# Kernel tuning notes

Measured on AMD Instinct MI355X. Metric: run time of the kernel, lower is better.

Reference implementation:

```python
import jax, jax.numpy as jnp
import numpy as np
from jax import lax

RPN_BBOX_STD_DEV = np.array([0.1, 0.1, 0.2, 0.2], dtype=np.float32)
PRE_NMS_LIMIT = 6000
PROPOSAL_COUNT = 1000
NMS_THRESHOLD = 0.7


def apply_box_deltas(boxes, deltas):
    # boxes: [N,4] (y1,x1,y2,x2); deltas: [N,4] (dy,dx,log dh,log dw)
    h = boxes[:, 2] - boxes[:, 0]
    w = boxes[:, 3] - boxes[:, 1]
    cy = boxes[:, 0] + 0.5 * h + deltas[:, 0] * h
    cx = boxes[:, 1] + 0.5 * w + deltas[:, 1] * w
    h = h * jnp.exp(deltas[:, 2])
    w = w * jnp.exp(deltas[:, 3])
    y1 = cy - 0.5 * h
    x1 = cx - 0.5 * w
    return jnp.stack([y1, x1, y1 + h, x1 + w], axis=1)


def pairwise_iou(boxes):
    # boxes: [N,4] -> iou [N,N]
    y1, x1, y2, x2 = boxes[:, 0], boxes[:, 1], boxes[:, 2], boxes[:, 3]
    area = (y2 - y1) * (x2 - x1)
    iy1 = jnp.maximum(y1[:, None], y1[None, :])
    ix1 = jnp.maximum(x1[:, None], x1[None, :])
    iy2 = jnp.minimum(y2[:, None], y2[None, :])
    ix2 = jnp.minimum(x2[:, None], x2[None, :])
    inter = jnp.maximum(iy2 - iy1, 0.0) * jnp.maximum(ix2 - ix1, 0.0)
    union = area[:, None] + area[None, :] - inter
    return inter / jnp.maximum(union, 1e-12)


def nms_keep_mask(boxes, iou_threshold):
    # boxes are sorted by descending score; greedy suppression.
    n = boxes.shape[0]
    iou = pairwise_iou(boxes)  # [N,N]
    idxs = jnp.arange(n)

    def body(i, keep):
        suppressed = jnp.any((iou[i] > iou_threshold) & keep & (idxs < i))
        return keep.at[i].set(jnp.logical_not(suppressed))

    return lax.fori_loop(0, n, body, jnp.zeros((n,), dtype=bool))


def proposal_single(scores, deltas, anchors):
    # scores: [A], deltas: [A,4], anchors: [A,4] -- single image
    top_scores, ix = lax.top_k(scores, PRE_NMS_LIMIT)           # sorted desc
    d = deltas[ix] * RPN_BBOX_STD_DEV[None, :]
    boxes = apply_box_deltas(anchors[ix], d)
    boxes = jnp.clip(boxes, 0.0, 1.0)                           # window [0,0,1,1]
    keep = lax.stop_gradient(nms_keep_mask(boxes, NMS_THRESHOLD))
    # select top PROPOSAL_COUNT kept boxes in score order, pad with zeros
    masked = jnp.where(keep, top_scores, -jnp.inf)
    _, sel = lax.top_k(masked, PROPOSAL_COUNT)
    valid = keep[sel]
    props = jnp.where(valid[:, None], boxes[sel], 0.0)          # [P,4]
    return props


def reference(rpn_probs, rpn_bbox, anchors):
    scores = rpn_probs[:, :, 1]  # fg prob
    return jax.vmap(proposal_single)(scores, rpn_bbox, anchors)


def setup_inputs() -> dict:
    key = jax.random.key(0)
    k1, k2, k3, k4 = jax.random.split(key, 4)
    B, A = 8, 131072
    rpn_probs = jax.random.uniform(k1, (B, A, 2), dtype=jnp.float32)
    rpn_bbox = jax.random.normal(k2, (B, A, 4), dtype=jnp.float32)
    # valid normalized anchors: y1<y2, x1<x2, inside [0,1]
    tl = jax.random.uniform(k3, (B, A, 2), dtype=jnp.float32) * 0.9
    wh = jax.random.uniform(k4, (B, A, 2), dtype=jnp.float32) * 0.1 + 1e-3
    anchors = jnp.concatenate([tl, tl + wh], axis=-1)
    return {"rpn_probs": rpn_probs, "rpn_bbox": rpn_bbox, "anchors": anchors}
```

## Files before the change

### kernel.cpp

```cpp
#include <hip/hip_runtime.h>

#pragma clang fp contract(off)

typedef unsigned long long u64;
typedef unsigned int u32;
typedef unsigned short u16;

#define BATCH 8
#define NA 131072
#define NSEL 6000
#define NT 24
#define TILE 256
#define NWORD (NT * 4)
#define NPAD (NT * TILE)
#define CAND_CAP 8192
#define PROP 1000
#define SCAP 4096
#define LDSE 12288
#define CELLCAP 256
#define LARGECAP 1024
#define LTHR 0.125f

#define OFF_HIST     0
#define OFF_BFILL    8256
#define OFF_SCNT     16512
#define OFF_CELLCNT  17344
#define MEMSET_BYTES 19456
#define OFF_TILET    19456
#define OFF_CAND     1592320
#define OFF_BOXES    2116608
#define OFF_CELLLIST 2903040
#define OFF_LARGE    3165184
#define OFF_SENT     3181568

__device__ __forceinline__ int bucket_of(u32 bits) {
  u32 hi = bits >> 16;
  if (hi >= 0x3E80u && hi < 0x3F80u) return (int)(hi - 0x3E80u);
  if (hi >= 0x3F80u && hi < 0x8000u) return 255;
  return -1;
}

__device__ __forceinline__ bool iou_gt(float4 A, float4 B, float areaA, float areaB) {
  float iy = fminf(A.z, B.z) - fmaxf(A.x, B.x);
  float ix = fminf(A.w, B.w) - fmaxf(A.y, B.y);
  float inter = fmaxf(iy, 0.0f) * fmaxf(ix, 0.0f);
  float uni = (areaA + areaB) - inter;
  float uc = fmaxf(uni, 1e-12f);
  return (double)inter >= 0x1.666667p-1 * (double)uc;
}

__device__ __forceinline__ void emit_pair(int b, int ra, int rb, u64* tileT,
                                          u32* sent, int* scnt) {
  int src = min(ra, rb), dst = max(ra, rb);
  int tsrc = src >> 8, tdst = dst >> 8;
  if (tsrc == tdst) {
    atomicOr(&tileT[(((size_t)b * NT + tdst) * TILE + (dst & 255)) * 4 + ((src >> 6) & 3)],
             1ULL << (src & 63));
  } else {
    int e = atomicAdd(&scnt[b * NT + tdst], 1);
    if (e < SCAP)
      sent[(size_t)(b * NT + tdst) * SCAP + e] = ((u32)src << 8) | (u32)(dst & 255);
  }
}

__device__ __forceinline__ u64 shfl_xor_u64(u64 v, int lanemask) {
  u32 lo = (u32)v, hi = (u32)(v >> 32);
  lo = (u32)__shfl_xor((int)lo, lanemask);
  hi = (u32)__shfl_xor((int)hi, lanemask);
  return ((u64)hi << 32) | (u64)lo;
}

__device__ __forceinline__ u64 valid_mask(int g) {
  int lo = g * 64;
  if (lo + 64 <= NSEL) return ~0ULL;
  if (lo >= NSEL) return 0ULL;
  return (1ULL << (NSEL - lo)) - 1ULL;
}

__device__ __forceinline__ void prefix_from_hist(const int* __restrict__ hist, int b,
                                                 int* h, int* bst, int* tb_s) {
  if (threadIdx.x < 256) h[threadIdx.x] = hist[b * 257 + threadIdx.x];
  __syncthreads();
  if (threadIdx.x == 0) {
    int run = 0, t = 0;
    bool found = false;
    for (int v = 255; v >= 0; --v) {
      bst[v] = run;
      run += h[v];
      if (!found && run >= NSEL) { t = v; found = true; }
    }
    *tb_s = t;
  }
  __syncthreads();
}

__global__ __launch_bounds__(256) void hist_kernel(const float* __restrict__ probs,
                                                   int* __restrict__ hist) {
  int b = blockIdx.y;
  const float2* p2 = reinterpret_cast<const float2*>(probs);
  __shared__ int h[257];
  for (int i = threadIdx.x; i < 257; i += 256) h[i] = 0;
  __syncthreads();
  int stride = gridDim.x * blockDim.x;
  for (int a = blockIdx.x * blockDim.x + threadIdx.x; a < NA; a += stride) {
    float sc = p2[(size_t)b * NA + a].y;
    int bk = bucket_of(__float_as_uint(sc));
    atomicAdd(&h[bk < 0 ? 256 : bk], 1);
  }
  __syncthreads();
  for (int i = threadIdx.x; i < 257; i += 256)
    if (h[i]) atomicAdd(&hist[b * 257 + i], h[i]);
}

__global__ __launch_bounds__(256) void gather_kernel(const float* __restrict__ probs,
                                                     const int* __restrict__ hist,
                                                     int* __restrict__ bfill,
                                                     u64* __restrict__ cand) {
  int b = blockIdx.y;
  const float2* p2 = reinterpret_cast<const float2*>(probs);
  __shared__ int h[256];
  __shared__ int bst[256];
  __shared__ int tb_s;
  prefix_from_hist(hist, b, h, bst, &tb_s);
  int tb = tb_s;
  int stride = gridDim.x * blockDim.x;
  for (int a = blockIdx.x * blockDim.x + threadIdx.x; a < NA; a += stride) {
    float sc = p2[(size_t)b * NA + a].y;
    u32 bits = __float_as_uint(sc);
    int bk = bucket_of(bits);
    if (bk >= tb) {
      int pos = bst[bk] + atomicAdd(&bfill[b * 257 + bk], 1);
      if (pos < CAND_CAP)
        cand[(size_t)b * CAND_CAP + pos] = ((u64)bits << 32) | (u64)(0xFFFFFFFFu - (u32)a);
    }
  }
}

__global__ __launch_bounds__(256) void sortdecode_kernel(const int* __restrict__ hist,
                                                         const int* __restrict__ bfill,
                                                         const u64* __restrict__ cand,
                                                         const float* __restrict__ anchors,
                                                         const float* __restrict__ deltas,
                                                         float4* __restrict__ boxes,
                                                         int* __restrict__ cellCnt,
                                                         u16* __restrict__ cellList,
                                                         u16* __restrict__ largeList,
                                                         u64* __restrict__ tileT) {
  int b = blockIdx.y;
  int tid = threadIdx.x;
  for (int g = blockIdx.x * 256 + tid; g < NT * TILE * 4; g += 64 * 256)
    tileT[(size_t)b * (NT * TILE * 4) + g] = 0ULL;
  __shared__ int h[256];
  __shared__ int bst[256];
  __shared__ int tb_s;
  prefix_from_hist(hist, b, h, bst, &tb_s);
  if (blockIdx.x == 0) {
    float4 z = {0.f, 0.f, 0.f, 0.f};
    for (int r = NSEL + tid; r < NPAD; r += 256) boxes[(size_t)b * NPAD + r] = z;
  }
  int v = tb_s + blockIdx.x;
  if (v > 255) return;
  int start = bst[v];
  if (start >= NSEL) return;
  int cnt = min(min(bfill[b * 257 + v], 1024), CAND_CAP - start);
  if (cnt <= 0) return;
  const u64* seg = cand + (size_t)b * CAND_CAP + start;
  __shared__ u64 s[1024];
  u64 x[4];
#pragma unroll
  for (int p = 0; p < 4; ++p) {
    int i = p * 256 + tid;
    x[p] = (i < cnt) ? seg[i] : 0ULL;
  }
  for (int k = 2; k <= 64; k <<= 1) {
    for (int j = k >> 1; j >= 1; j >>= 1) {
#pragma unroll
      for (int p = 0; p < 4; ++p) {
        int i = p * 256 + tid;
        u64 pv = shfl_xor_u64(x[p], j);
        bool takemax = (((i & j) == 0) == ((i & k) == 0));
        u64 mx = x[p] > pv ? x[p] : pv;
        u64 mn = x[p] < pv ? x[p] : pv;
        x[p] = takemax ? mx : mn;
      }
    }
  }
#pragma unroll
  for (int p = 0; p < 4; ++p) s[p * 256 + tid] = x[p];
  __syncthreads();
  for (int k = 128; k <= 1024; k <<= 1) {
    for (int j = k >> 1; j >= 64; j >>= 1) {
      for (int q = tid; q < 512; q += 256) {
        int i = ((q & ~(j - 1)) << 1) | (q & (j - 1));
        int ixj = i | j;
        u64 a = s[i], c = s[ixj];
        bool up = ((i & k) == 0);
        if (up ? (a < c) : (a > c)) { s[i] = c; s[ixj] = a; }
      }
      __syncthreads();
    }
#pragma unroll
    for (int p = 0; p < 4; ++p) x[p] = s[p * 256 + tid];
    for (int j = 32; j >= 1; j >>= 1) {
#pragma unroll
      for (int p = 0; p < 4; ++p) {
        int i = p * 256 + tid;
        u64 pv = shfl_xor_u64(x[p], j);
        bool takemax = (((i & j) == 0) == ((i & k) == 0));
        u64 mx = x[p] > pv ? x[p] : pv;
        u64 mn = x[p] < pv ? x[p] : pv;
        x[p] = takemax ? mx : mn;
      }
    }
    __syncthreads();
#pragma unroll
    for (int p = 0; p < 4; ++p) s[p * 256 + tid] = x[p];
    __syncthreads();
  }
  for (int i = tid; i < cnt; i += 256) {
    int r = start + i;
    if (r >= NSEL) continue;
    u64 key = s[i];
    float4 o = {0.f, 0.f, 0.f, 0.f};
    u32 idx = 0xFFFFFFFFu - (u32)(key & 0xFFFFFFFFu);
    if (idx < NA) {
      float4 av = *reinterpret_cast<const float4*>(anchors + ((size_t)b * NA + idx) * 4);
      float4 dv = *reinterpret_cast<const float4*>(deltas + ((size_t)b * NA + idx) * 4);
      float y1 = av.x, x1 = av.y, y2 = av.z, x2 = av.w;
      float dy = dv.x * 0.1f, dx = dv.y * 0.1f;
      float dh = dv.z * 0.2f, dw = dv.w * 0.2f;
      float hh = y2 - y1, ww = x2 - x1;
      float cy = y1 + 0.5f * hh + dy * hh;
      float cx = x1 + 0.5f * ww + dx * ww;
      hh = hh * expf(dh);
      ww = ww * expf(dw);
      float ny1 = cy - 0.5f * hh, nx1 = cx - 0.5f * ww;
      float ny2 = ny1 + hh, nx2 = nx1 + ww;
      o.x = fminf(fmaxf(ny1, 0.f), 1.f);
      o.y = fminf(fmaxf(nx1, 0.f), 1.f);
      o.z = fminf(fmaxf(ny2, 0.f), 1.f);
      o.w = fminf(fmaxf(nx2, 0.f), 1.f);
    }
    boxes[(size_t)b * NPAD + r] = o;
    float bh = o.z - o.x, bw = o.w - o.y;
    if (bh > LTHR || bw > LTHR) {
      int pos = atomicAdd(&cellCnt[b * 65 + 64], 1);
      if (pos < LARGECAP) largeList[b * LARGECAP + pos] = (u16)r;
    } else {
      int gy = min(7, max(0, (int)((o.x + o.z) * 4.0f)));
      int gx = min(7, max(0, (int)((o.y + o.w) * 4.0f)));
      int cell = gy * 8 + gx;
      int pos = atomicAdd(&cellCnt[b * 65 + cell], 1);
      if (pos < CELLCAP) cellList[((size_t)b * 64 + cell) * CELLCAP + pos] = (u16)r;
    }
  }
}

__global__ __launch_bounds__(256) void pairs_kernel(const float4* __restrict__ boxes,
                                                    const u16* __restrict__ cellList,
                                                    const u16* __restrict__ largeList,
                                                    const int* __restrict__ cellCnt,
                                                    u64* __restrict__ tileT,
                                                    u32* __restrict__ sent,
                                                    int* __restrict__ scnt) {
  int b = blockIdx.y;
  int tid = threadIdx.x;
  if (blockIdx.x >= 64) {
    int lb = blockIdx.x - 64;
    int nL = min(cellCnt[b * 65 + 64], LARGECAP);
    if (nL == 0) return;
    for (int li = lb; li < nL; li += 64) {
      int L = largeList[b * LARGECAP + li];
      float4 Lb = boxes[(size_t)b * NPAD + L];
      float hL = Lb.z - Lb.x, wL = Lb.w - Lb.y;
      if (0.7f * hL >= 0.126f || 0.7f * wL >= 0.126f) continue;
      float La = hL * wL;
      float sLy = Lb.x + Lb.z, sLx = Lb.y + Lb.w;
      int gy0 = max(0, (int)((sLy - 0.08f) * 4.0f));
      int gy1 = min(7, (int)((sLy + 0.08f) * 4.0f));
      int gx0 = max(0, (int)((sLx - 0.08f) * 4.0f));
      int gx1 = min(7, (int)((sLx + 0.08f) * 4.0f));
      for (int gy = gy0; gy <= gy1; ++gy)
        for (int gx = gx0; gx <= gx1; ++gx) {
          int cc = gy * 8 + gx;
          int cnt = min(cellCnt[b * 65 + cc], CELLCAP);
          for (int i = tid; i < cnt; i += 256) {
            int r = cellList[((size_t)b * 64 + cc) * CELLCAP + i];
            float4 jb = boxes[(size_t)b * NPAD + r];
            float ja = (jb.z - jb.x) * (jb.w - jb.y);
            if (iou_gt(Lb, jb, La, ja)) emit_pair(b, L, r, tileT, sent, scnt);
          }
        }
    }
    int s = 1;
    while ((1 << s) < nL) ++s;
    int tot = nL << s, m = (1 << s) - 1;
    int stride = 64 * 256;
    for (int t = lb * 256 + tid; t < tot; t += stride) {
      int i = t >> s, j = t & m;
      if (j >= nL || i >= j) continue;
      int Li = largeList[b * LARGECAP + i];
      int Lj = largeList[b * LARGECAP + j];
      float4 A = boxes[(size_t)b * NPAD + Li];
      float4 B = boxes[(size_t)b * NPAD + Lj];
      float aA = (A.z - A.x) * (A.w - A.y);
      float aB = (B.z - B.x) * (B.w - B.y);
      if (iou_gt(A, B, aA, aB)) emit_pair(b, Li, Lj, tileT, sent, scnt);
    }
    return;
  }
  int c = blockIdx.x;
  int cy = c >> 3, cx = c & 7;
  int nA = min(cellCnt[b * 65 + c], CELLCAP);
  if (nA == 0) return;
  __shared__ float4 Ab[CELLCAP];
  __shared__ float Aa[CELLCAP];
  __shared__ float Asx[CELLCAP];
  __shared__ float Asy[CELLCAP];
  __shared__ u16 Ai[CELLCAP];
  __shared__ u16 fAi[CELLCAP];
  __shared__ float4 Bb[3 * CELLCAP];
  __shared__ float Ba[3 * CELLCAP];
  __shared__ u16 Bi[3 * CELLCAP];
  __shared__ int nfA_s, nfB_s;
  for (int i = tid; i < nA; i += 256) {
    int r = cellList[((size_t)b * 64 + c) * CELLCAP + i];
    float4 bx = boxes[(size_t)b * NPAD + r];
    Ab[i] = bx;
    Aa[i] = (bx.z - bx.x) * (bx.w - bx.y);
    Asy[i] = bx.x + bx.z;
    Asx[i] = bx.y + bx.w;
    Ai[i] = (u16)r;
  }
  __syncthreads();
  {
    int totS = (nA * (nA - 1)) >> 1;
    for (int t = tid; t < totS; t += 256) {
      int i = (int)((1.0f + sqrtf(8.0f * (float)t + 1.0f)) * 0.5f);
      int tri = (i * (i - 1)) >> 1;
      if (t < tri) {
        --i;
        tri = (i * (i - 1)) >> 1;
      } else if (t >= tri + i) {
        tri += i;
        ++i;
      }
      int j = t - tri;
      if (iou_gt(Ab[i], Ab[j], Aa[i], Aa[j]))
        emit_pair(b, Ai[i], Ai[j], tileT, sent, scnt);
    }
  }
  if (cx < 7) {
    __syncthreads();
    if (tid == 0) { nfA_s = 0; nfB_s = 0; }
    __syncthreads();
    float XR2 = (float)(cx + 1) * 0.25f;
    for (int i = tid; i < nA; i += 256)
      if (Asx[i] > XR2 - 0.078f) fAi[atomicAdd(&nfA_s, 1)] = (u16)i;
    int nc = c + 1;
    int nN = min(cellCnt[b * 65 + nc], CELLCAP);
    for (int i = tid; i < nN; i += 256) {
      int r = cellList[((size_t)b * 64 + nc) * CELLCAP + i];
      float4 bx = boxes[(size_t)b * NPAD + r];
      if (bx.y + bx.w < XR2 + 0.078f) {
        int p = atomicAdd(&nfB_s, 1);
        Bb[p] = bx;
        Ba[p] = (bx.z - bx.x) * (bx.w - bx.y);
        Bi[p] = (u16)r;
      }
    }
    __syncthreads();
    int nfA = nfA_s, nfB = nfB_s;
    if (nfA && nfB) {
      int s = 1;
      while ((1 << s) < nfB) ++s;
      int tot = nfA << s, m = (1 << s) - 1;
      for (int t = tid; t < tot; t += 256) {
        int ii = fAi[t >> s], j = t & m;
        if (j < nfB && iou_gt(Ab[ii], Bb[j], Aa[ii], Ba[j]))
          emit_pair(b, Ai[ii], Bi[j], tileT, sent, scnt);
      }
    }
  }
  if (cy < 7) {
    __syncthreads();
    if (tid == 0) { nfA_s = 0; nfB_s = 0; }
    __syncthreads();
    float YB2 = (float)(cy + 1) * 0.25f;
    float XL2 = (float)cx * 0.25f;
    float XR2 = (float)(cx + 1) * 0.25f;
    for (int i = tid; i < nA; i += 256)
      if (Asy[i] > YB2 - 0.078f) fAi[atomicAdd(&nfA_s, 1)] = (u16)i;
    for (int k = 0; k < 3; ++k) {
      int nx = cx + k - 1;
      if (nx < 0 || nx > 7) continue;
      int nc = (cy + 1) * 8 + nx;
      int nN = min(cellCnt[b * 65 + nc], CELLCAP);
      for (int i = tid; i < nN; i += 256) {
        int r = cellList[((size_t)b * 64 + nc) * CELLCAP + i];
        float4 bx = boxes[(size_t)b * NPAD + r];
        float bsy = bx.x + bx.z, bsx = bx.y + bx.w;
        bool ok = bsy < YB2 + 0.078f;
        if (k == 0) ok = ok && (bsx > XL2 - 0.078f);
        if (k == 2) ok = ok && (bsx < XR2 + 0.078f);
        if (ok) {
          int p = atomicAdd(&nfB_s, 1);
          Bb[p] = bx;
          Ba[p] = (bx.z - bx.x) * (bx.w - bx.y);
          Bi[p] = (u16)r;
        }
      }
    }
    __syncthreads();
    int nfA = nfA_s, nfB = nfB_s;
    if (nfA && nfB) {
      int s = 1;
      while ((1 << s) < nfB) ++s;
      int tot = nfA << s, m = (1 << s) - 1;
      for (int t = tid; t < tot; t += 256) {
        int ii = fAi[t >> s], j = t & m;
        if (j < nfB && iou_gt(Ab[ii], Bb[j], Aa[ii], Ba[j]))
          emit_pair(b, Ai[ii], Bi[j], tileT, sent, scnt);
      }
    }
  }
}

__global__ __launch_bounds__(512) void nms_kernel(const u32* __restrict__ sent,
                                                  const int* __restrict__ scnt,
                                                  const u64* __restrict__ tileT,
                                                  const float4* __restrict__ boxes,
                                                  float4* __restrict__ out) {
  int b = blockIdx.x;
  int tid = threadIdx.x;
  int lane = tid & 63;
  int wv = tid >> 6;
  __shared__ u32 entS[LDSE];
  __shared__ u32 rmb[TILE];
  __shared__ u64 Kall[NWORD];
  __shared__ int cw[NT];
  __shared__ int prefix[NT + 1];
  __shared__ int baseT[NT];
  if (tid < NT) cw[tid] = min(scnt[b * NT + tid], SCAP);
  if (tid < TILE) rmb[tid] = 0u;
  if (tid < NWORD) Kall[tid] = 0ULL;
  {
    float4 z = {0.f, 0.f, 0.f, 0.f};
    for (int i = tid; i < PROP; i += 512) out[(size_t)b * PROP + i] = z;
  }
  __syncthreads();
  if (tid == 0) {
    int run = 0;
    for (int t = 0; t < NT; ++t) { prefix[t] = run; run += cw[t]; }
    prefix[NT] = run;
  }
  __syncthreads();
  for (int t = wv; t < NT; t += 8) {
    const u32* gb = sent + (size_t)(b * NT + t) * SCAP;
    int base = prefix[t], n = cw[t];
    for (int e = lane; e < n; e += 64) {
      int slot = base + e;
      if (slot < LDSE) entS[slot] = gb[e];
    }
  }
  __syncthreads();
  if (wv == 0) {
    const u64* tb0 = tileT + (size_t)b * (NT * TILE * 4);
    u64 mc[4][4], mn[4][4];
#pragma unroll
    for (int q = 0; q < 4; ++q)
#pragma unroll
      for (int j = 0; j < 4; ++j)
        mc[q][j] = tb0[(size_t)(q * 64 + lane) * 4 + j];
    int total = 0;
    for (int t = 0; t < NT; ++t) {
      if (t + 1 < NT) {
        const u64* nb = tb0 + (size_t)(t + 1) * (TILE * 4);
#pragma unroll
        for (int q = 0; q < 4; ++q)
#pragma unroll
          for (int j = 0; j < 4; ++j)
            mn[q][j] = nb[(size_t)(q * 64 + lane) * 4 + j];
      }
      {
        int n = cw[t], base = prefix[t];
        for (int e = lane; e < n; e += 64) {
          int slot = base + e;
          u32 ent = (slot < LDSE) ? entS[slot] : sent[(size_t)(b * NT + t) * SCAP + e];
          int srcr = (int)(ent >> 8);
          if ((Kall[srcr >> 6] >> (srcr & 63)) & 1ULL) rmb[ent & 255] = 1u;
        }
      }
      u32 f0 = rmb[lane], f1 = rmb[64 + lane], f2 = rmb[128 + lane], f3 = rmb[192 + lane];
      rmb[lane] = 0u;
      rmb[64 + lane] = 0u;
      rmb[128 + lane] = 0u;
      rmb[192 + lane] = 0u;
      int gw = t * 4;
      u64 K0, K1, K2, K3;
      {
        bool alive0 = (f0 == 0u) && ((valid_mask(gw) >> lane) & 1ULL);
        u64 cm = mc[0][0];
        u64 K = __ballot(alive0);
        for (int it = 0; it < 70; ++it) {
          bool alive = alive0 && ((K & cm) == 0ULL);
          u64 Kn = __ballot(alive);
          if (Kn == K) break;
          K = Kn;
        }
        K0 = K;
      }
      {
        u64 pre = K0 & mc[1][0];
        bool alive0 = (f1 == 0u) && ((valid_mask(gw + 1) >> lane) & 1ULL) && (pre == 0ULL);
        u64 cm = mc[1][1];
        u64 K = __ballot(alive0);
        for (int it = 0; it < 70; ++it) {
          bool alive = alive0 && ((K & cm) == 0ULL);
          u64 Kn = __ballot(alive);
          if (Kn == K) break;
          K = Kn;
        }
        K1 = K;
      }
      {
        u64 pre = (K0 & mc[2][0]) | (K1 & mc[2][1]);
        bool alive0 = (f2 == 0u) && ((valid_mask(gw + 2) >> lane) & 1ULL) && (pre == 0ULL);
        u64 cm = mc[2][2];
        u64 K = __ballot(alive0);
        for (int it = 0; it < 70; ++it) {
          bool alive = alive0 && ((K & cm) == 0ULL);
          u64 Kn = __ballot(alive);
          if (Kn == K) break;
          K = Kn;
        }
        K2 = K;
      }
      {
        u64 pre = (K0 & mc[3][0]) | (K1 & mc[3][1]) | (K2 & mc[3][2]);
        bool alive0 = (f3 == 0u) && ((valid_mask(gw + 3) >> lane) & 1ULL) && (pre == 0ULL);
        u64 cm = mc[3][3];
        u64 K = __ballot(alive0);
        for (int it = 0; it < 70; ++it) {
          bool alive = alive0 && ((K & cm) == 0ULL);
          u64 Kn = __ballot(alive);
          if (Kn == K) break;
          K = Kn;
        }
        K3 = K;
      }
      if (lane == 0) {
        Kall[gw] = K0;
        Kall[gw + 1] = K1;
        Kall[gw + 2] = K2;
        Kall[gw + 3] = K3;
        baseT[t] = total;
      }
      total += __popcll(K0) + __popcll(K1) + __popcll(K2) + __popcll(K3);
#pragma unroll
      for (int q = 0; q < 4; ++q)
#pragma unroll
        for (int j = 0; j < 4; ++j)
          mc[q][j] = mn[q][j];
    }
  }
  __syncthreads();
  for (int i = tid; i < NSEL; i += 512) {
    int g = i >> 6, bb = i & 63;
    u64 K = Kall[g];
    if ((K >> bb) & 1ULL) {
      int t = i >> 8;
      int rank = baseT[t];
      for (int q = t * 4; q < g; ++q) rank += __popcll(Kall[q]);
      rank += __popcll(K & ((1ULL << bb) - 1ULL));
      if (rank < PROP) out[(size_t)b * PROP + rank] = boxes[(size_t)b * NPAD + i];
    }
  }
}

extern "C" void kernel_launch(void* const* d_in, const int* in_sizes, int n_in,
                              void* d_out, int out_size, void* d_ws, size_t ws_size,
                              hipStream_t stream) {
  const float* probs = (const float*)d_in[0];
  const float* deltas = (const float*)d_in[1];
  const float* anchors = (const float*)d_in[2];
  char* ws = (char*)d_ws;
  int* hist = (int*)(ws + OFF_HIST);
  int* bfill = (int*)(ws + OFF_BFILL);
  int* scnt = (int*)(ws + OFF_SCNT);
  int* cellCnt = (int*)(ws + OFF_CELLCNT);
  u64* tileT = (u64*)(ws + OFF_TILET);
  u64* cand = (u64*)(ws + OFF_CAND);
  float4* boxes = (float4*)(ws + OFF_BOXES);
  u16* cellList = (u16*)(ws + OFF_CELLLIST);
  u16* largeList = (u16*)(ws + OFF_LARGE);
  u32* sent = (u32*)(ws + OFF_SENT);

  (void)hipMemsetAsync(ws, 0, MEMSET_BYTES, stream);

  hist_kernel<<<dim3(64, BATCH), 256, 0, stream>>>(probs, hist);
  gather_kernel<<<dim3(64, BATCH), 256, 0, stream>>>(probs, hist, bfill, cand);
  sortdecode_kernel<<<dim3(64, BATCH), 256, 0, stream>>>(hist, bfill, cand, anchors,
                                                         deltas, boxes, cellCnt,
                                                         cellList, largeList, tileT);
  pairs_kernel<<<dim3(128, BATCH), 256, 0, stream>>>(boxes, cellList, largeList,
                                                     cellCnt, tileT, sent, scnt);
  nms_kernel<<<BATCH, 512, 0, stream>>>(sent, scnt, tileT, boxes, (float4*)d_out);
}
```

Before: 218.8 us.

## Fuse histogram, gather, sort-decode and pair stages into one persistent kernel

Merges four kernels into a single persistent launch of 512 blocks. The stages are separated by software grid barriers built on agent-scope atomics. Score bits are kept in registers between the histogram and gather stages, so probs is read once instead of twice, and the serial per-bucket prefix is replaced with a parallel suffix scan. The aim is to remove launch gaps and the extra global read. In exchange the pairs stage now uses half as many blocks, and correctness depends on all 512 blocks being resident at once.

```diff
diff --git a/kernel.cpp b/kernel.cpp
--- a/kernel.cpp
+++ b/kernel.cpp
@@ -20,18 +20,20 @@
 #define CELLCAP 256
 #define LARGECAP 1024
 #define LTHR 0.125f
+#define NBLK 512
 
 #define OFF_HIST     0
 #define OFF_BFILL    8256
 #define OFF_SCNT     16512
 #define OFF_CELLCNT  17344
-#define MEMSET_BYTES 19456
-#define OFF_TILET    19456
-#define OFF_CAND     1592320
-#define OFF_BOXES    2116608
-#define OFF_CELLLIST 2903040
-#define OFF_LARGE    3165184
-#define OFF_SENT     3181568
+#define OFF_BAR      19456
+#define MEMSET_BYTES 19520
+#define OFF_TILET    19520
+#define OFF_CAND     1592384
+#define OFF_BOXES    2116672
+#define OFF_CELLLIST 2903104
+#define OFF_LARGE    3165248
+#define OFF_SENT     3181632
 
 __device__ __forceinline__ int bucket_of(u32 bits) {
   u32 hi = bits >> 16;
@@ -77,350 +79,378 @@
   return (1ULL << (NSEL - lo)) - 1ULL;
 }
 
-__device__ __forceinline__ void prefix_from_hist(const int* __restrict__ hist, int b,
-                                                 int* h, int* bst, int* tb_s) {
-  if (threadIdx.x < 256) h[threadIdx.x] = hist[b * 257 + threadIdx.x];
+__device__ __forceinline__ void grid_barrier(int* bar, int idx) {
   __syncthreads();
   if (threadIdx.x == 0) {
-    int run = 0, t = 0;
-    bool found = false;
-    for (int v = 255; v >= 0; --v) {
-      bst[v] = run;
-      run += h[v];
-      if (!found && run >= NSEL) { t = v; found = true; }
-    }
-    *tb_s = t;
-  }
-  __syncthreads();
-}
-
-__global__ __launch_bounds__(256) void hist_kernel(const float* __restrict__ probs,
-                                                   int* __restrict__ hist) {
-  int b = blockIdx.y;
+    __threadfence();
+    int a = __hip_atomic_fetch_add(&bar[idx * 2], 1, __ATOMIC_ACQ_REL,
+                                   __HIP_MEMORY_SCOPE_AGENT);
+    if (a == NBLK - 1) {
+      __hip_atomic_store(&bar[idx * 2 + 1], 1, __ATOMIC_RELEASE,
+                         __HIP_MEMORY_SCOPE_AGENT);
+    } else {
+      while (!__hip_atomic_load(&bar[idx * 2 + 1], __ATOMIC_ACQUIRE,
+                                __HIP_MEMORY_SCOPE_AGENT))
+        __builtin_amdgcn_s_sleep(2);
+    }
+    __threadfence();
+  }
+  __syncthreads();
+}
+
+__device__ __forceinline__ void prefix_scan(const int* __restrict__ hist, int b,
+                                            int* h, int* suf, int* bst, int* tb_s) {
+  int tid = threadIdx.x;
+  int v = hist[b * 257 + tid];
+  h[tid] = v;
+  suf[tid] = v;
+  if (tid == 0) *tb_s = 0;
+  __syncthreads();
+  for (int d = 1; d < 256; d <<= 1) {
+    int add = (tid + d < 256) ? suf[tid + d] : 0;
+    __syncthreads();
+    suf[tid] += add;
+    __syncthreads();
+  }
+  bst[tid] = suf[tid] - h[tid];
+  if (suf[tid] >= NSEL && (tid == 255 || suf[tid + 1] < NSEL)) *tb_s = tid;
+  __syncthreads();
+}
+
+#define SMEM_BYTES 25600
+
+__global__ __launch_bounds__(256, 4) void mega_kernel(
+    const float* __restrict__ probs, int* __restrict__ hist,
+    int* __restrict__ bfill, u64* __restrict__ cand,
+    const float* __restrict__ anchors, const float* __restrict__ deltas,
+    float4* __restrict__ boxes, int* __restrict__ cellCnt,
+    u16* __restrict__ cellList, u16* __restrict__ largeList,
+    u64* __restrict__ tileT, u32* __restrict__ sent, int* __restrict__ scnt,
+    int* __restrict__ bar) {
+  __shared__ __attribute__((aligned(16))) char smraw[SMEM_BYTES];
+  int bid = blockIdx.x;
+  int tid = threadIdx.x;
+  int b = bid >> 6, sub = bid & 63;
   const float2* p2 = reinterpret_cast<const float2*>(probs);
-  __shared__ int h[257];
-  for (int i = threadIdx.x; i < 257; i += 256) h[i] = 0;
-  __syncthreads();
-  int stride = gridDim.x * blockDim.x;
-  for (int a = blockIdx.x * blockDim.x + threadIdx.x; a < NA; a += stride) {
-    float sc = p2[(size_t)b * NA + a].y;
-    int bk = bucket_of(__float_as_uint(sc));
-    atomicAdd(&h[bk < 0 ? 256 : bk], 1);
-  }
-  __syncthreads();
-  for (int i = threadIdx.x; i < 257; i += 256)
-    if (h[i]) atomicAdd(&hist[b * 257 + i], h[i]);
-}
-
-__global__ __launch_bounds__(256) void gather_kernel(const float* __restrict__ probs,
-                                                     const int* __restrict__ hist,
-                                                     int* __restrict__ bfill,
-                                                     u64* __restrict__ cand) {
-  int b = blockIdx.y;
-  const float2* p2 = reinterpret_cast<const float2*>(probs);
-  __shared__ int h[256];
-  __shared__ int bst[256];
-  __shared__ int tb_s;
-  prefix_from_hist(hist, b, h, bst, &tb_s);
-  int tb = tb_s;
-  int stride = gridDim.x * blockDim.x;
-  for (int a = blockIdx.x * blockDim.x + threadIdx.x; a < NA; a += stride) {
-    float sc = p2[(size_t)b * NA + a].y;
-    u32 bits = __float_as_uint(sc);
+
+  for (size_t g = (size_t)bid * 256 + tid; g < (size_t)BATCH * NT * TILE * 4;
+       g += (size_t)NBLK * 256)
+    tileT[g] = 0ULL;
+  int* h0 = (int*)smraw;
+  for (int i = tid; i < 257; i += 256) h0[i] = 0;
+  __syncthreads();
+  u32 cbits[8];
+  int abase = sub * 2048;
+#pragma unroll
+  for (int k = 0; k < 8; ++k) {
+    int a = abase + k * 256 + tid;
+    u32 bits = __float_as_uint(p2[(size_t)b * NA + a].y);
+    cbits[k] = bits;
     int bk = bucket_of(bits);
-    if (bk >= tb) {
-      int pos = bst[bk] + atomicAdd(&bfill[b * 257 + bk], 1);
-      if (pos < CAND_CAP)
-        cand[(size_t)b * CAND_CAP + pos] = ((u64)bits << 32) | (u64)(0xFFFFFFFFu - (u32)a);
-    }
-  }
-}
-
-__global__ __launch_bounds__(256) void sortdecode_kernel(const int* __restrict__ hist,
-                                                         const int* __restrict__ bfill,
-                                                         const u64* __restrict__ cand,
-                                                         const float* __restrict__ anchors,
-                                                         const float* __restrict__ deltas,
-                                                         float4* __restrict__ boxes,
-                                                         int* __restrict__ cellCnt,
-                                                         u16* __restrict__ cellList,
-                                                         u16* __restrict__ largeList,
-                                                         u64* __restrict__ tileT) {
-  int b = blockIdx.y;
-  int tid = threadIdx.x;
-  for (int g = blockIdx.x * 256 + tid; g < NT * TILE * 4; g += 64 * 256)
-    tileT[(size_t)b * (NT * TILE * 4) + g] = 0ULL;
-  __shared__ int h[256];
-  __shared__ int bst[256];
-  __shared__ int tb_s;
-  prefix_from_hist(hist, b, h, bst, &tb_s);
-  if (blockIdx.x == 0) {
-    float4 z = {0.f, 0.f, 0.f, 0.f};
-    for (int r = NSEL + tid; r < NPAD; r += 256) boxes[(size_t)b * NPAD + r] = z;
-  }
-  int v = tb_s + blockIdx.x;
-  if (v > 255) return;
-  int start = bst[v];
-  if (start >= NSEL) return;
-  int cnt = min(min(bfill[b * 257 + v], 1024), CAND_CAP - start);
-  if (cnt <= 0) return;
-  const u64* seg = cand + (size_t)b * CAND_CAP + start;
-  __shared__ u64 s[1024];
-  u64 x[4];
-#pragma unroll
-  for (int p = 0; p < 4; ++p) {
-    int i = p * 256 + tid;
-    x[p] = (i < cnt) ? seg[i] : 0ULL;
-  }
-  for (int k = 2; k <= 64; k <<= 1) {
-    for (int j = k >> 1; j >= 1; j >>= 1) {
+    atomicAdd(&h0[bk < 0 ? 256 : bk], 1);
+  }
+  __syncthreads();
+  for (int i = tid; i < 257; i += 256)
+    if (h0[i]) atomicAdd(&hist[b * 257 + i], h0[i]);
+  grid_barrier(bar, 0);
+
+  {
+    int* h = (int*)smraw;
+    int* suf = (int*)(smraw + 1024);
+    int* bst = (int*)(smraw + 2048);
+    int* tbp = (int*)(smraw + 3072);
+    prefix_scan(hist, b, h, suf, bst, tbp);
+    int tb = *tbp;
+#pragma unroll
+    for (int k = 0; k < 8; ++k) {
+      u32 bits = cbits[k];
+      int bk = bucket_of(bits);
+      if (bk >= tb) {
+        int a = abase + k * 256 + tid;
+        int pos = bst[bk] + atomicAdd(&bfill[b * 257 + bk], 1);
+        if (pos < CAND_CAP)
+          cand[(size_t)b * CAND_CAP + pos] =
+              ((u64)bits << 32) | (u64)(0xFFFFFFFFu - (u32)a);
+      }
+    }
+  }
+  grid_barrier(bar, 1);
+
+  {
+    int* h = (int*)smraw;
+    int* suf = (int*)(smraw + 1024);
+    int* bst = (int*)(smraw + 2048);
+    int* tbp = (int*)(smraw + 3072);
+    u64* s = (u64*)(smraw + 3088);
+    prefix_scan(hist, b, h, suf, bst, tbp);
+    int tb = *tbp;
+    if (sub == 0) {
+      float4 z = {0.f, 0.f, 0.f, 0.f};
+      for (int r = NSEL + tid; r < NPAD; r += 256) boxes[(size_t)b * NPAD + r] = z;
+    }
+    int v = tb + sub;
+    bool active = (v <= 255);
+    int start = 0, cnt = 0;
+    if (active) {
+      start = bst[v];
+      active = (start < NSEL);
+    }
+    if (active) {
+      cnt = min(min(bfill[b * 257 + v], 1024), CAND_CAP - start);
+      active = (cnt > 0);
+    }
+    if (active) {
+      const u64* seg = cand + (size_t)b * CAND_CAP + start;
+      u64 x[4];
 #pragma unroll
       for (int p = 0; p < 4; ++p) {
         int i = p * 256 + tid;
-        u64 pv = shfl_xor_u64(x[p], j);
-        bool takemax = (((i & j) == 0) == ((i & k) == 0));
-        u64 mx = x[p] > pv ? x[p] : pv;
-        u64 mn = x[p] < pv ? x[p] : pv;
-        x[p] = takemax ? mx : mn;
-      }
-    }
-  }
-#pragma unroll
-  for (int p = 0; p < 4; ++p) s[p * 256 + tid] = x[p];
-  __syncthreads();
-  for (int k = 128; k <= 1024; k <<= 1) {
-    for (int j = k >> 1; j >= 64; j >>= 1) {
-      for (int q = tid; q < 512; q += 256) {
-        int i = ((q & ~(j - 1)) << 1) | (q & (j - 1));
-        int ixj = i | j;
-        u64 a = s[i], c = s[ixj];
-        bool up = ((i & k) == 0);
-        if (up ? (a < c) : (a > c)) { s[i] = c; s[ixj] = a; }
-      }
+        x[p] = (i < cnt) ? seg[i] : 0ULL;
+      }
+      for (int k = 2; k <= 64; k <<= 1) {
+        for (int j = k >> 1; j >= 1; j >>= 1) {
+#pragma unroll
+          for (int p = 0; p < 4; ++p) {
+            int i = p * 256 + tid;
+            u64 pv = shfl_xor_u64(x[p], j);
+            bool takemax = (((i & j) == 0) == ((i & k) == 0));
+            u64 mx = x[p] > pv ? x[p] : pv;
+            u64 mn = x[p] < pv ? x[p] : pv;
+            x[p] = takemax ? mx : mn;
+          }
+        }
+      }
+#pragma unroll
+      for (int p = 0; p < 4; ++p) s[p * 256 + tid] = x[p];
       __syncthreads();
-    }
-#pragma unroll
-    for (int p = 0; p < 4; ++p) x[p] = s[p * 256 + tid];
-    for (int j = 32; j >= 1; j >>= 1) {
-#pragma unroll
-      for (int p = 0; p < 4; ++p) {
-        int i = p * 256 + tid;
-        u64 pv = shfl_xor_u64(x[p], j);
-        bool takemax = (((i & j) == 0) == ((i & k) == 0));
-        u64 mx = x[p] > pv ? x[p] : pv;
-        u64 mn = x[p] < pv ? x[p] : pv;
-        x[p] = takemax ? mx : mn;
-      }
-    }
-    __syncthreads();
-#pragma unroll
-    for (int p = 0; p < 4; ++p) s[p * 256 + tid] = x[p];
-    __syncthreads();
-  }
-  for (int i = tid; i < cnt; i += 256) {
-    int r = start + i;
-    if (r >= NSEL) continue;
-    u64 key = s[i];
-    float4 o = {0.f, 0.f, 0.f, 0.f};
-    u32 idx = 0xFFFFFFFFu - (u32)(key & 0xFFFFFFFFu);
-    if (idx < NA) {
-      float4 av = *reinterpret_cast<const float4*>(anchors + ((size_t)b * NA + idx) * 4);
-      float4 dv = *reinterpret_cast<const float4*>(deltas + ((size_t)b * NA + idx) * 4);
-      float y1 = av.x, x1 = av.y, y2 = av.z, x2 = av.w;
-      float dy = dv.x * 0.1f, dx = dv.y * 0.1f;
-      float dh = dv.z * 0.2f, dw = dv.w * 0.2f;
-      float hh = y2 - y1, ww = x2 - x1;
-      float cy = y1 + 0.5f * hh + dy * hh;
-      float cx = x1 + 0.5f * ww + dx * ww;
-      hh = hh * expf(dh);
-      ww = ww * expf(dw);
-      float ny1 = cy - 0.5f * hh, nx1 = cx - 0.5f * ww;
-      float ny2 = ny1 + hh, nx2 = nx1 + ww;
-      o.x = fminf(fmaxf(ny1, 0.f), 1.f);
-      o.y = fminf(fmaxf(nx1, 0.f), 1.f);
-      o.z = fminf(fmaxf(ny2, 0.f), 1.f);
-      o.w = fminf(fmaxf(nx2, 0.f), 1.f);
-    }
-    boxes[(size_t)b * NPAD + r] = o;
-    float bh = o.z - o.x, bw = o.w - o.y;
-    if (bh > LTHR || bw > LTHR) {
-      int pos = atomicAdd(&cellCnt[b * 65 + 64], 1);
-      if (pos < LARGECAP) largeList[b * LARGECAP + pos] = (u16)r;
-    } else {
-      int gy = min(7, max(0, (int)((o.x + o.z) * 4.0f)));
-      int gx = min(7, max(0, (int)((o.y + o.w) * 4.0f)));
-      int cell = gy * 8 + gx;
-      int pos = atomicAdd(&cellCnt[b * 65 + cell], 1);
-      if (pos < CELLCAP) cellList[((size_t)b * 64 + cell) * CELLCAP + pos] = (u16)r;
-    }
-  }
-}
-
-__global__ __launch_bounds__(256) void pairs_kernel(const float4* __restrict__ boxes,
-                                                    const u16* __restrict__ cellList,
-                                                    const u16* __restrict__ largeList,
-                                                    const int* __restrict__ cellCnt,
-                                                    u64* __restrict__ tileT,
-                                                    u32* __restrict__ sent,
-                                                    int* __restrict__ scnt) {
-  int b = blockIdx.y;
-  int tid = threadIdx.x;
-  if (blockIdx.x >= 64) {
-    int lb = blockIdx.x - 64;
+      for (int k = 128; k <= 1024; k <<= 1) {
+        for (int j = k >> 1; j >= 64; j >>= 1) {
+          for (int q = tid; q < 512; q += 256) {
+            int i = ((q & ~(j - 1)) << 1) | (q & (j - 1));
+            int ixj = i | j;
+            u64 a = s[i], c = s[ixj];
+            bool up = ((i & k) == 0);
+            if (up ? (a < c) : (a > c)) { s[i] = c; s[ixj] = a; }
+          }
+          __syncthreads();
+        }
+#pragma unroll
+        for (int p = 0; p < 4; ++p) x[p] = s[p * 256 + tid];
+        for (int j = 32; j >= 1; j >>= 1) {
+#pragma unroll
+          for (int p = 0; p < 4; ++p) {
+            int i = p * 256 + tid;
+            u64 pv = shfl_xor_u64(x[p], j);
+            bool takemax = (((i & j) == 0) == ((i & k) == 0));
+            u64 mx = x[p] > pv ? x[p] : pv;
+            u64 mn = x[p] < pv ? x[p] : pv;
+            x[p] = takemax ? mx : mn;
+          }
+        }
+        __syncthreads();
+#pragma unroll
+        for (int p = 0; p < 4; ++p) s[p * 256 + tid] = x[p];
+        __syncthreads();
+      }
+      for (int i = tid; i < cnt; i += 256) {
+        int r = start + i;
+        if (r >= NSEL) continue;
+        u64 key = s[i];
+        float4 o = {0.f, 0.f, 0.f, 0.f};
+        u32 idx = 0xFFFFFFFFu - (u32)(key & 0xFFFFFFFFu);
+        if (idx < NA) {
+          float4 av = *reinterpret_cast<const float4*>(anchors + ((size_t)b * NA + idx) * 4);
+          float4 dv = *reinterpret_cast<const float4*>(deltas + ((size_t)b * NA + idx) * 4);
+          float y1 = av.x, x1 = av.y, y2 = av.z, x2 = av.w;
+          float dy = dv.x * 0.1f, dx = dv.y * 0.1f;
+          float dh = dv.z * 0.2f, dw = dv.w * 0.2f;
+          float hh = y2 - y1, ww = x2 - x1;
+          float cy = y1 + 0.5f * hh + dy * hh;
+          float cx = x1 + 0.5f * ww + dx * ww;
+          hh = hh * expf(dh);
+          ww = ww * expf(dw);
+          float ny1 = cy - 0.5f * hh, nx1 = cx - 0.5f * ww;
+          float ny2 = ny1 + hh, nx2 = nx1 + ww;
+          o.x = fminf(fmaxf(ny1, 0.f), 1.f);
+          o.y = fminf(fmaxf(nx1, 0.f), 1.f);
+          o.z = fminf(fmaxf(ny2, 0.f), 1.f);
+          o.w = fminf(fmaxf(nx2, 0.f), 1.f);
+        }
+        boxes[(size_t)b * NPAD + r] = o;
+        float bh = o.z - o.x, bw = o.w - o.y;
+        if (bh > LTHR || bw > LTHR) {
+          int pos = atomicAdd(&cellCnt[b * 65 + 64], 1);
+          if (pos < LARGECAP) largeList[b * LARGECAP + pos] = (u16)r;
+        } else {
+          int gy = min(7, max(0, (int)((o.x + o.z) * 4.0f)));
+          int gx = min(7, max(0, (int)((o.y + o.w) * 4.0f)));
+          int cell = gy * 8 + gx;
+          int pos = atomicAdd(&cellCnt[b * 65 + cell], 1);
+          if (pos < CELLCAP) cellList[((size_t)b * 64 + cell) * CELLCAP + pos] = (u16)r;
+        }
+      }
+    }
+  }
+  grid_barrier(bar, 2);
+
+  {
+    float4* Ab = (float4*)smraw;
+    float* Aa = (float*)(smraw + 4096);
+    float* Asx = (float*)(smraw + 5120);
+    float* Asy = (float*)(smraw + 6144);
+    u16* Ai = (u16*)(smraw + 7168);
+    u16* fAi = (u16*)(smraw + 7680);
+    float4* Bb = (float4*)(smraw + 8192);
+    float* Ba = (float*)(smraw + 20480);
+    u16* Bi = (u16*)(smraw + 23552);
+    int* nfA_s = (int*)(smraw + 25088);
+    int* nfB_s = (int*)(smraw + 25092);
+
+    int c = sub;
+    int cy = c >> 3, cx = c & 7;
+    int nA = min(cellCnt[b * 65 + c], CELLCAP);
+    if (nA > 0) {
+      for (int i = tid; i < nA; i += 256) {
+        int r = cellList[((size_t)b * 64 + c) * CELLCAP + i];
+        float4 bx = boxes[(size_t)b * NPAD + r];
+        Ab[i] = bx;
+        Aa[i] = (bx.z - bx.x) * (bx.w - bx.y);
+        Asy[i] = bx.x + bx.z;
+        Asx[i] = bx.y + bx.w;
+        Ai[i] = (u16)r;
+      }
+      __syncthreads();
+      {
+        int totS = (nA * (nA - 1)) >> 1;
+        for (int t = tid; t < totS; t += 256) {
+          int i = (int)((1.0f + sqrtf(8.0f * (float)t + 1.0f)) * 0.5f);
+          int tri = (i * (i - 1)) >> 1;
+          if (t < tri) {
+            --i;
+            tri = (i * (i - 1)) >> 1;
+          } else if (t >= tri + i) {
+            tri += i;
+            ++i;
+          }
+          int j = t - tri;
+          if (iou_gt(Ab[i], Ab[j], Aa[i], Aa[j]))
+            emit_pair(b, Ai[i], Ai[j], tileT, sent, scnt);
+        }
+      }
+      if (cx < 7) {
+        __syncthreads();
+        if (tid == 0) { *nfA_s = 0; *nfB_s = 0; }
+        __syncthreads();
+        float XR2 = (float)(cx + 1) * 0.25f;
+        for (int i = tid; i < nA; i += 256)
+          if (Asx[i] > XR2 - 0.078f) fAi[atomicAdd(nfA_s, 1)] = (u16)i;
+        int nc = c + 1;
+        int nN = min(cellCnt[b * 65 + nc], CELLCAP);
+        for (int i = tid; i < nN; i += 256) {
+          int r = cellList[((size_t)b * 64 + nc) * CELLCAP + i];
+          float4 bx = boxes[(size_t)b * NPAD + r];
+          if (bx.y + bx.w < XR2 + 0.078f) {
+            int p = atomicAdd(nfB_s, 1);
+            Bb[p] = bx;
+            Ba[p] = (bx.z - bx.x) * (bx.w - bx.y);
+            Bi[p] = (u16)r;
+          }
+        }
+        __syncthreads();
+        int nfA = *nfA_s, nfB = *nfB_s;
+        if (nfA && nfB) {
+          int s = 1;
+          while ((1 << s) < nfB) ++s;
+          int tot = nfA << s, m = (1 << s) - 1;
+          for (int t = tid; t < tot; t += 256) {
+            int ii = fAi[t >> s], j = t & m;
+            if (j < nfB && iou_gt(Ab[ii], Bb[j], Aa[ii], Ba[j]))
+              emit_pair(b, Ai[ii], Bi[j], tileT, sent, scnt);
+          }
+        }
+      }
+      if (cy < 7) {
+        __syncthreads();
+        if (tid == 0) { *nfA_s = 0; *nfB_s = 0; }
+        __syncthreads();
+        float YB2 = (float)(cy + 1) * 0.25f;
+        float XL2 = (float)cx * 0.25f;
+        float XR2 = (float)(cx + 1) * 0.25f;
+        for (int i = tid; i < nA; i += 256)
+          if (Asy[i] > YB2 - 0.078f) fAi[atomicAdd(nfA_s, 1)] = (u16)i;
+        for (int k = 0; k < 3; ++k) {
+          int nx = cx + k - 1;
+          if (nx < 0 || nx > 7) continue;
+          int nc = (cy + 1) * 8 + nx;
+          int nN = min(cellCnt[b * 65 + nc], CELLCAP);
+          for (int i = tid; i < nN; i += 256) {
+            int r = cellList[((size_t)b * 64 + nc) * CELLCAP + i];
+            float4 bx = boxes[(size_t)b * NPAD + r];
+            float bsy = bx.x + bx.z, bsx = bx.y + bx.w;
+            bool ok = bsy < YB2 + 0.078f;
+            if (k == 0) ok = ok && (bsx > XL2 - 0.078f);
+            if (k == 2) ok = ok && (bsx < XR2 + 0.078f);
+            if (ok) {
+              int p = atomicAdd(nfB_s, 1);
+              Bb[p] = bx;
+              Ba[p] = (bx.z - bx.x) * (bx.w - bx.y);
+              Bi[p] = (u16)r;
+            }
+          }
+        }
+        __syncthreads();
+        int nfA = *nfA_s, nfB = *nfB_s;
+        if (nfA && nfB) {
+          int s = 1;
+          while ((1 << s) < nfB) ++s;
+          int tot = nfA << s, m = (1 << s) - 1;
+          for (int t = tid; t < tot; t += 256) {
+            int ii = fAi[t >> s], j = t & m;
+            if (j < nfB && iou_gt(Ab[ii], Bb[j], Aa[ii], Ba[j]))
+              emit_pair(b, Ai[ii], Bi[j], tileT, sent, scnt);
+          }
+        }
+      }
+    }
     int nL = min(cellCnt[b * 65 + 64], LARGECAP);
-    if (nL == 0) return;
-    for (int li = lb; li < nL; li += 64) {
-      int L = largeList[b * LARGECAP + li];
-      float4 Lb = boxes[(size_t)b * NPAD + L];
-      float hL = Lb.z - Lb.x, wL = Lb.w - Lb.y;
-      if (0.7f * hL >= 0.126f || 0.7f * wL >= 0.126f) continue;
-      float La = hL * wL;
-      float sLy = Lb.x + Lb.z, sLx = Lb.y + Lb.w;
-      int gy0 = max(0, (int)((sLy - 0.08f) * 4.0f));
-      int gy1 = min(7, (int)((sLy + 0.08f) * 4.0f));
-      int gx0 = max(0, (int)((sLx - 0.08f) * 4.0f));
-      int gx1 = min(7, (int)((sLx + 0.08f) * 4.0f));
-      for (int gy = gy0; gy <= gy1; ++gy)
-        for (int gx = gx0; gx <= gx1; ++gx) {
-          int cc = gy * 8 + gx;
-          int cnt = min(cellCnt[b * 65 + cc], CELLCAP);
-          for (int i = tid; i < cnt; i += 256) {
-            int r = cellList[((size_t)b * 64 + cc) * CELLCAP + i];
-            float4 jb = boxes[(size_t)b * NPAD + r];
-            float ja = (jb.z - jb.x) * (jb.w - jb.y);
-            if (iou_gt(Lb, jb, La, ja)) emit_pair(b, L, r, tileT, sent, scnt);
-          }
-        }
-    }
-    int s = 1;
-    while ((1 << s) < nL) ++s;
-    int tot = nL << s, m = (1 << s) - 1;
-    int stride = 64 * 256;
-    for (int t = lb * 256 + tid; t < tot; t += stride) {
-      int i = t >> s, j = t & m;
-      if (j >= nL || i >= j) continue;
-      int Li = largeList[b * LARGECAP + i];
-      int Lj = largeList[b * LARGECAP + j];
-      float4 A = boxes[(size_t)b * NPAD + Li];
-      float4 B = boxes[(size_t)b * NPAD + Lj];
-      float aA = (A.z - A.x) * (A.w - A.y);
-      float aB = (B.z - B.x) * (B.w - B.y);
-      if (iou_gt(A, B, aA, aB)) emit_pair(b, Li, Lj, tileT, sent, scnt);
-    }
-    return;
-  }
-  int c = blockIdx.x;
-  int cy = c >> 3, cx = c & 7;
-  int nA = min(cellCnt[b * 65 + c], CELLCAP);
-  if (nA == 0) return;
-  __shared__ float4 Ab[CELLCAP];
-  __shared__ float Aa[CELLCAP];
-  __shared__ float Asx[CELLCAP];
-  __shared__ float Asy[CELLCAP];
-  __shared__ u16 Ai[CELLCAP];
-  __shared__ u16 fAi[CELLCAP];
-  __shared__ float4 Bb[3 * CELLCAP];
-  __shared__ float Ba[3 * CELLCAP];
-  __shared__ u16 Bi[3 * CELLCAP];
-  __shared__ int nfA_s, nfB_s;
-  for (int i = tid; i < nA; i += 256) {
-    int r = cellList[((size_t)b * 64 + c) * CELLCAP + i];
-    float4 bx = boxes[(size_t)b * NPAD + r];
-    Ab[i] = bx;
-    Aa[i] = (bx.z - bx.x) * (bx.w - bx.y);
-    Asy[i] = bx.x + bx.z;
-    Asx[i] = bx.y + bx.w;
-    Ai[i] = (u16)r;
-  }
-  __syncthreads();
-  {
-    int totS = (nA * (nA - 1)) >> 1;
-    for (int t = tid; t < totS; t += 256) {
-      int i = (int)((1.0f + sqrtf(8.0f * (float)t + 1.0f)) * 0.5f);
-      int tri = (i * (i - 1)) >> 1;
-      if (t < tri) {
-        --i;
-        tri = (i * (i - 1)) >> 1;
-      } else if (t >= tri + i) {
-        tri += i;
-        ++i;
-      }
-      int j = t - tri;
-      if (iou_gt(Ab[i], Ab[j], Aa[i], Aa[j]))
-        emit_pair(b, Ai[i], Ai[j], tileT, sent, scnt);
-    }
-  }
-  if (cx < 7) {
-    __syncthreads();
-    if (tid == 0) { nfA_s = 0; nfB_s = 0; }
-    __syncthreads();
-    float XR2 = (float)(cx + 1) * 0.25f;
-    for (int i = tid; i < nA; i += 256)
-      if (Asx[i] > XR2 - 0.078f) fAi[atomicAdd(&nfA_s, 1)] = (u16)i;
-    int nc = c + 1;
-    int nN = min(cellCnt[b * 65 + nc], CELLCAP);
-    for (int i = tid; i < nN; i += 256) {
-      int r = cellList[((size_t)b * 64 + nc) * CELLCAP + i];
-      float4 bx = boxes[(size_t)b * NPAD + r];
-      if (bx.y + bx.w < XR2 + 0.078f) {
-        int p = atomicAdd(&nfB_s, 1);
-        Bb[p] = bx;
-        Ba[p] = (bx.z - bx.x) * (bx.w - bx.y);
-        Bi[p] = (u16)r;
-      }
-    }
-    __syncthreads();
-    int nfA = nfA_s, nfB = nfB_s;
-    if (nfA && nfB) {
+    if (nL > 0) {
+      for (int li = sub; li < nL; li += 64) {
+        int L = largeList[b * LARGECAP + li];
+        float4 Lb = boxes[(size_t)b * NPAD + L];
+        float hL = Lb.z - Lb.x, wL = Lb.w - Lb.y;
+        if (0.7f * hL >= 0.126f || 0.7f * wL >= 0.126f) continue;
+        float La = hL * wL;
+        float sLy = Lb.x + Lb.z, sLx = Lb.y + Lb.w;
+        int gy0 = max(0, (int)((sLy - 0.08f) * 4.0f));
+        int gy1 = min(7, (int)((sLy + 0.08f) * 4.0f));
+        int gx0 = max(0, (int)((sLx - 0.08f) * 4.0f));
+        int gx1 = min(7, (int)((sLx + 0.08f) * 4.0f));
+        for (int gy = gy0; gy <= gy1; ++gy)
+          for (int gx = gx0; gx <= gx1; ++gx) {
+            int cc = gy * 8 + gx;
+            int cnt2 = min(cellCnt[b * 65 + cc], CELLCAP);
+            for (int i = tid; i < cnt2; i += 256) {
+              int r = cellList[((size_t)b * 64 + cc) * CELLCAP + i];
+              float4 jb = boxes[(size_t)b * NPAD + r];
+              float ja = (jb.z - jb.x) * (jb.w - jb.y);
+              if (iou_gt(Lb, jb, La, ja)) emit_pair(b, L, r, tileT, sent, scnt);
+            }
+          }
+      }
       int s = 1;
-      while ((1 << s) < nfB) ++s;
-      int tot = nfA << s, m = (1 << s) - 1;
-      for (int t = tid; t < tot; t += 256) {
-        int ii = fAi[t >> s], j = t & m;
-        if (j < nfB && iou_gt(Ab[ii], Bb[j], Aa[ii], Ba[j]))
-          emit_pair(b, Ai[ii], Bi[j], tileT, sent, scnt);
-      }
-    }
-  }
-  if (cy < 7) {
-    __syncthreads();
-    if (tid == 0) { nfA_s = 0; nfB_s = 0; }
-    __syncthreads();
-    float YB2 = (float)(cy + 1) * 0.25f;
-    float XL2 = (float)cx * 0.25f;
-    float XR2 = (float)(cx + 1) * 0.25f;
-    for (int i = tid; i < nA; i += 256)
-      if (Asy[i] > YB2 - 0.078f) fAi[atomicAdd(&nfA_s, 1)] = (u16)i;
-    for (int k = 0; k < 3; ++k) {
-      int nx = cx + k - 1;
-      if (nx < 0 || nx > 7) continue;
-      int nc = (cy + 1) * 8 + nx;
-      int nN = min(cellCnt[b * 65 + nc], CELLCAP);
-      for (int i = tid; i < nN; i += 256) {
-        int r = cellList[((size_t)b * 64 + nc) * CELLCAP + i];
-        float4 bx = boxes[(size_t)b * NPAD + r];
-        float bsy = bx.x + bx.z, bsx = bx.y + bx.w;
-        bool ok = bsy < YB2 + 0.078f;
-        if (k == 0) ok = ok && (bsx > XL2 - 0.078f);
-        if (k == 2) ok = ok && (bsx < XR2 + 0.078f);
-        if (ok) {
-          int p = atomicAdd(&nfB_s, 1);
-          Bb[p] = bx;
-          Ba[p] = (bx.z - bx.x) * (bx.w - bx.y);
-          Bi[p] = (u16)r;
-        }
-      }
-    }
-    __syncthreads();
-    int nfA = nfA_s, nfB = nfB_s;
-    if (nfA && nfB) {
-      int s = 1;
-      while ((1 << s) < nfB) ++s;
-      int tot = nfA << s, m = (1 << s) - 1;
-      for (int t = tid; t < tot; t += 256) {
-        int ii = fAi[t >> s], j = t & m;
-        if (j < nfB && iou_gt(Ab[ii], Bb[j], Aa[ii], Ba[j]))
-          emit_pair(b, Ai[ii], Bi[j], tileT, sent, scnt);
+      while ((1 << s) < nL) ++s;
+      int tot = nL << s, m = (1 << s) - 1;
+      int stride = 64 * 256;
+      for (int t = sub * 256 + tid; t < tot; t += stride) {
+        int i = t >> s, j = t & m;
+        if (j >= nL || i >= j) continue;
+        int Li = largeList[b * LARGECAP + i];
+        int Lj = largeList[b * LARGECAP + j];
+        float4 A = boxes[(size_t)b * NPAD + Li];
+        float4 B = boxes[(size_t)b * NPAD + Lj];
+        float aA = (A.z - A.x) * (A.w - A.y);
+        float aB = (B.z - B.x) * (B.w - B.y);
+        if (iou_gt(A, B, aA, aB)) emit_pair(b, Li, Lj, tileT, sent, scnt);
       }
     }
   }
@@ -589,6 +619,7 @@
   int* bfill = (int*)(ws + OFF_BFILL);
   int* scnt = (int*)(ws + OFF_SCNT);
   int* cellCnt = (int*)(ws + OFF_CELLCNT);
+  int* bar = (int*)(ws + OFF_BAR);
   u64* tileT = (u64*)(ws + OFF_TILET);
   u64* cand = (u64*)(ws + OFF_CAND);
   float4* boxes = (float4*)(ws + OFF_BOXES);
@@ -598,12 +629,8 @@
 
   (void)hipMemsetAsync(ws, 0, MEMSET_BYTES, stream);
 
-  hist_kernel<<<dim3(64, BATCH), 256, 0, stream>>>(probs, hist);
-  gather_kernel<<<dim3(64, BATCH), 256, 0, stream>>>(probs, hist, bfill, cand);
-  sortdecode_kernel<<<dim3(64, BATCH), 256, 0, stream>>>(hist, bfill, cand, anchors,
-                                                         deltas, boxes, cellCnt,
-                                                         cellList, largeList, tileT);
-  pairs_kernel<<<dim3(128, BATCH), 256, 0, stream>>>(boxes, cellList, largeList,
-                                                     cellCnt, tileT, sent, scnt);
+  mega_kernel<<<NBLK, 256, 0, stream>>>(probs, hist, bfill, cand, anchors, deltas,
+                                        boxes, cellCnt, cellList, largeList, tileT,
+                                        sent, scnt, bar);
   nms_kernel<<<BATCH, 512, 0, stream>>>(sent, scnt, tileT, boxes, (float4*)d_out);
 }
```

After: 378.6 us. 1.73x slower.
